# Kernel tuning notes

Measured on AMD Instinct MI355X. Metric: run time of the kernel, lower is better.

Reference implementation:

```python
import jax, jax.numpy as jnp
import numpy as np

DIM = 2048
HV = 32          # num value heads
HK = 16          # num key heads
DK = 128         # head_k_dim
DV = 128         # head_v_dim
KW = 4           # conv kernel width
KEY_DIM = HK * DK            # 2048
VAL_DIM = HV * DV            # 4096
CONV_DIM = 2 * KEY_DIM + VAL_DIM  # 8192
EPS = 1e-6
B, T = 2, 2048


def setup_inputs() -> dict:
    key = jax.random.key(0)
    ks = jax.random.split(key, 10)
    s = 0.02
    x = jax.random.normal(ks[0], (B, T, DIM), jnp.float32)
    W_qkv = jax.random.normal(ks[1], (DIM, CONV_DIM), jnp.float32) * s
    W_z = jax.random.normal(ks[2], (DIM, VAL_DIM), jnp.float32) * s
    W_a = jax.random.normal(ks[3], (DIM, HV), jnp.float32) * s
    W_b = jax.random.normal(ks[4], (DIM, HV), jnp.float32) * s
    W_out = jax.random.normal(ks[5], (VAL_DIM, DIM), jnp.float32) * s
    conv_w = jax.random.normal(ks[6], (CONV_DIM, KW), jnp.float32) * 0.2
    A_log = jnp.log(jax.random.uniform(ks[7], (HV,), jnp.float32, 1e-3, 16.0))
    dt_bias = jnp.ones((HV,), jnp.float32)
    norm_weight = jnp.ones((DV,), jnp.float32)
    return {"x": x, "W_qkv": W_qkv, "W_z": W_z, "W_a": W_a, "W_b": W_b,
            "W_out": W_out, "conv_w": conv_w, "dt_bias": dt_bias,
            "A_log": A_log, "norm_weight": norm_weight}


def _l2norm(t):
    return t * jax.lax.rsqrt(jnp.sum(t * t, axis=-1, keepdims=True) + EPS)


def _forward(x, W_qkv, W_z, W_a, W_b, W_out, conv_w, dt_bias, A_log, norm_weight):
    Bb, Tt, _ = x.shape
    mixed = x @ W_qkv                       # [B,T,CONV_DIM]
    z = x @ W_z                             # [B,T,VAL_DIM]
    a = x @ W_a                             # [B,T,HV]
    b = x @ W_b                             # [B,T,HV]

    # depthwise causal conv1d (left pad KW-1) + silu
    xp = jnp.pad(mixed, ((0, 0), (KW - 1, 0), (0, 0)))
    conv = sum(xp[:, i:i + Tt, :] * conv_w[:, i] for i in range(KW))
    mixed = jax.nn.silu(conv)

    q, k, v = jnp.split(mixed, [KEY_DIM, 2 * KEY_DIM], axis=-1)
    q = q.reshape(Bb, Tt, HK, DK)
    k = k.reshape(Bb, Tt, HK, DK)
    v = v.reshape(Bb, Tt, HV, DV)
    rep = HV // HK
    q = jnp.repeat(q, rep, axis=2)          # [B,T,HV,DK]
    k = jnp.repeat(k, rep, axis=2)

    # decay / beta
    beta = jax.nn.sigmoid(b)                                    # [B,T,HV]
    g = -jnp.exp(A_log) * jax.nn.softplus(a + dt_bias)          # [B,T,HV], < 0

    # qk l2norm in kernel + scale
    q = _l2norm(q) * (DK ** -0.5)
    k = _l2norm(k)

    # gated delta rule recurrence, time-major scan
    qT = q.transpose(1, 0, 2, 3)
    kT = k.transpose(1, 0, 2, 3)
    vT = v.transpose(1, 0, 2, 3)
    gT = g.transpose(1, 0, 2)
    bT = beta.transpose(1, 0, 2)
    S0 = jnp.zeros((Bb, HV, DK, DV), jnp.float32)

    def step(S, inp):
        qt, kt, vt, gt, bt = inp
        S = S * jnp.exp(gt)[..., None, None]
        pred = jnp.einsum('bhk,bhkv->bhv', kt, S)
        u = (vt - pred) * bt[..., None]
        S = S + jnp.einsum('bhk,bhv->bhkv', kt, u)
        o = jnp.einsum('bhk,bhkv->bhv', qt, S)
        return S, o

    _, oT = jax.lax.scan(step, S0, (qT, kT, vT, gT, bT))
    o = oT.transpose(1, 0, 2, 3)            # [B,T,HV,DV]

    # gated RMSNorm over head_v_dim: weight * rmsnorm(o) * silu(z)
    var = jnp.mean(o * o, axis=-1, keepdims=True)
    on = o * jax.lax.rsqrt(var + EPS) * norm_weight
    zg = z.reshape(Bb, Tt, HV, DV)
    on = on * jax.nn.silu(zg)

    return on.reshape(Bb, Tt, VAL_DIM) @ W_out


def reference(x, W_qkv, W_z, W_a, W_b, W_out, conv_w, dt_bias, A_log, norm_weight):
    return _forward(x, W_qkv, W_z, W_a, W_b, W_out, conv_w, dt_bias, A_log, norm_weight)
```

## Files before the change

### kernel.cpp

```cpp
#include <hip/hip_runtime.h>
#include <hip/hip_bf16.h>
#include <cstdint>
#include <cstddef>

#define DIM_ 2048
#define HV_ 32
#define HK_ 16
#define DK_ 128
#define DV_ 128
#define KW_ 4
#define KEY_DIM_ 2048
#define VAL_DIM_ 4096
#define CONV_DIM_ 8192
#define B_ 2
#define T_ 2048
#define BT_ 4096
#define CH_ 64
#define NC_ (T_ / CH_)

typedef short s8v __attribute__((ext_vector_type(8)));
typedef float f4v __attribute__((ext_vector_type(4)));

__device__ __forceinline__ unsigned short f2b(float f) {
    union { float f; unsigned u; } c; c.f = f;
    unsigned u = c.u;
    return (unsigned short)((u + 0x7fffu + ((u >> 16) & 1u)) >> 16);
}
__device__ __forceinline__ float b2f(unsigned short s) {
    union { unsigned u; float f; } c; c.u = ((unsigned)s) << 16;
    return c.f;
}
__device__ __forceinline__ unsigned int pk2(float a, float b) {
    return (unsigned)f2b(a) | ((unsigned)f2b(b) << 16);
}
__device__ __forceinline__ float silu(float x) { return x / (1.f + expf(-x)); }

__global__ void cast_bf16_k(const float* __restrict__ in, unsigned short* __restrict__ out, int n8) {
    int i = blockIdx.x * blockDim.x + threadIdx.x;
    if (i >= n8) return;
    int base = i * 8;
    f4v a = *(const f4v*)(in + base);
    f4v b = *(const f4v*)(in + base + 4);
    s8v o;
    o[0] = (short)f2b(a[0]); o[1] = (short)f2b(a[1]); o[2] = (short)f2b(a[2]); o[3] = (short)f2b(a[3]);
    o[4] = (short)f2b(b[0]); o[5] = (short)f2b(b[1]); o[6] = (short)f2b(b[2]); o[7] = (short)f2b(b[3]);
    *(s8v*)(out + base) = o;
}

__global__ void transpose_cast_k(const float* __restrict__ in, unsigned short* __restrict__ out,
                                 int R, int C) {
    __shared__ float tile[32][33];
    int c0 = blockIdx.x * 32, r0 = blockIdx.y * 32;
    int tx = threadIdx.x & 31, ty = threadIdx.x >> 5;
#pragma unroll
    for (int j = 0; j < 32; j += 8)
        tile[ty + j][tx] = in[(size_t)(r0 + ty + j) * C + c0 + tx];
    __syncthreads();
#pragma unroll
    for (int j = 0; j < 32; j += 8)
        out[(size_t)(c0 + ty + j) * R + r0 + tx] = f2b(tile[tx][ty + j]);
}

__global__ void pack_ab_k(const float* __restrict__ Wa, const float* __restrict__ Wb,
                          float* __restrict__ WabP) {
    int idx = blockIdx.x * 256 + threadIdx.x;
    int k = idx >> 6;
    int c = idx & 63;
    float v = (c < 32) ? Wa[(size_t)k * 32 + c] : Wb[(size_t)k * 32 + (c - 32)];
    WabP[((size_t)(k >> 2) * 64 + c) * 4 + (k & 3)] = v;
}

template <int OUT_BF16>
__global__ __launch_bounds__(256) void gemm_bt_k(const unsigned short* __restrict__ A,
                                                 const unsigned short* __restrict__ BT,
                                                 void* __restrict__ Cv,
                                                 int M, int N, int K) {
    __shared__ __attribute__((aligned(16))) unsigned short As[128 * 64];
    __shared__ __attribute__((aligned(16))) unsigned short Bs[128 * 64];
    const int tid = threadIdx.x;
    const int wid = tid >> 6, lane = tid & 63;
    const int wm = wid >> 1, wn = wid & 1;
    const int m0 = blockIdx.y * 128, n0 = blockIdx.x * 128;

    f4v acc[4][4];
#pragma unroll
    for (int i = 0; i < 4; i++)
#pragma unroll
        for (int j = 0; j < 4; j++) acc[i][j] = (f4v){0.f, 0.f, 0.f, 0.f};

    const int rowA = tid >> 3;
    const int cb   = (tid & 7) << 4;

    for (int kt = 0; kt < K; kt += 64) {
#pragma unroll
        for (int i = 0; i < 4; i++) {
            int row = i * 32 + rowA;
            int scb = cb ^ ((row & 7) << 4);
            const unsigned short* ga = A  + (size_t)(m0 + row) * K + kt + (scb >> 1);
            const unsigned short* gb = BT + (size_t)(n0 + row) * K + kt + (scb >> 1);
            char* la = (char*)As + i * 4096 + (wid << 10);
            char* lb = (char*)Bs + i * 4096 + (wid << 10);
            __builtin_amdgcn_global_load_lds(
                (const __attribute__((address_space(1))) unsigned int*)ga,
                (__attribute__((address_space(3))) unsigned int*)la, 16, 0, 0);
            __builtin_amdgcn_global_load_lds(
                (const __attribute__((address_space(1))) unsigned int*)gb,
                (__attribute__((address_space(3))) unsigned int*)lb, 16, 0, 0);
        }
        __syncthreads();
#pragma unroll
        for (int kk = 0; kk < 2; kk++) {
            s8v af[4], bfr[4];
#pragma unroll
            for (int mi = 0; mi < 4; mi++) {
                int row = wm * 64 + mi * 16 + (lane & 15);
                int byteoff = (row << 7) + ((kk * 64 + ((lane >> 4) << 4)) ^ ((row & 7) << 4));
                af[mi] = *(const s8v*)((const char*)As + byteoff);
            }
#pragma unroll
            for (int ni = 0; ni < 4; ni++) {
                int row = wn * 64 + ni * 16 + (lane & 15);
                int byteoff = (row << 7) + ((kk * 64 + ((lane >> 4) << 4)) ^ ((row & 7) << 4));
                bfr[ni] = *(const s8v*)((const char*)Bs + byteoff);
            }
#pragma unroll
            for (int mi = 0; mi < 4; mi++)
#pragma unroll
                for (int ni = 0; ni < 4; ni++)
                    acc[mi][ni] = __builtin_amdgcn_mfma_f32_16x16x32_bf16(
                        af[mi], bfr[ni], acc[mi][ni], 0, 0, 0);
        }
        __syncthreads();
    }
#pragma unroll
    for (int mi = 0; mi < 4; mi++) {
#pragma unroll
        for (int ni = 0; ni < 4; ni++) {
            int row = m0 + wm * 64 + mi * 16 + ((lane >> 4) << 2);
            int col = n0 + wn * 64 + ni * 16 + (lane & 15);
#pragma unroll
            for (int r = 0; r < 4; r++) {
                float v = acc[mi][ni][r];
                if (OUT_BF16)
                    ((unsigned short*)Cv)[(size_t)(row + r) * N + col] = f2b(v);
                else
                    ((float*)Cv)[(size_t)(row + r) * N + col] = v;
            }
        }
    }
}

__global__ __launch_bounds__(256) void ab_gbeta_k(const float* __restrict__ x,
                                                  const float* __restrict__ WabP,
                                                  const float* __restrict__ dt_bias,
                                                  const float* __restrict__ A_log,
                                                  float* __restrict__ g, float* __restrict__ beta) {
    const int c = threadIdx.x & 63;
    const int rg = __builtin_amdgcn_readfirstlane(threadIdx.x >> 6);
    const int row = blockIdx.x * 4 + rg;
    const float* xp = x + (size_t)row * 2048;
    const float* wp = WabP + c * 4;
    float acc0 = 0.f, acc1 = 0.f;
#pragma unroll 4
    for (int kb = 0; kb < 512; kb += 2) {
        f4v w0 = *(const f4v*)(wp + (size_t)kb * 256);
        f4v w1 = *(const f4v*)(wp + (size_t)(kb + 1) * 256);
        f4v x0 = *(const f4v*)(xp + kb * 4);
        f4v x1 = *(const f4v*)(xp + kb * 4 + 4);
        acc0 += x0[0] * w0[0] + x0[1] * w0[1] + x0[2] * w0[2] + x0[3] * w0[3];
        acc1 += x1[0] * w1[0] + x1[1] * w1[1] + x1[2] * w1[2] + x1[3] * w1[3];
    }
    float tot = acc0 + acc1;
    if (c < 32) {
        float av = tot + dt_bias[c];
        float sp = (av > 20.f) ? av : log1pf(expf(av));
        g[(size_t)row * 32 + c] = -expf(A_log[c]) * sp;
    } else {
        beta[(size_t)row * 32 + (c - 32)] = 1.f / (1.f + expf(-tot));
    }
}

__global__ __launch_bounds__(256) void conv_fused_k(const unsigned short* __restrict__ mixp,
                                                    const float* __restrict__ convw,
                                                    unsigned short* __restrict__ qn,
                                                    unsigned short* __restrict__ kn,
                                                    unsigned short* __restrict__ vv) {
    int btid = blockIdx.x;
    int t = btid & (T_ - 1);
    int c = (blockIdx.y << 9) + (threadIdx.x << 1);
    const unsigned short* base = mixp + (size_t)btid * CONV_DIM_ + c;
    unsigned m3 = *(const unsigned*)(base);
    unsigned m2 = (t >= 1) ? *(const unsigned*)(base - CONV_DIM_) : 0u;
    unsigned m1 = (t >= 2) ? *(const unsigned*)(base - 2 * CONV_DIM_) : 0u;
    unsigned m0 = (t >= 3) ? *(const unsigned*)(base - 3 * CONV_DIM_) : 0u;
    f4v w0 = *(const f4v*)(convw + (size_t)c * 4);
    f4v w1 = *(const f4v*)(convw + (size_t)c * 4 + 4);
    float v0 = b2f((unsigned short)(m3 & 0xffff)) * w0[3] + b2f((unsigned short)(m2 & 0xffff)) * w0[2]
             + b2f((unsigned short)(m1 & 0xffff)) * w0[1] + b2f((unsigned short)(m0 & 0xffff)) * w0[0];
    float v1 = b2f((unsigned short)(m3 >> 16)) * w1[3] + b2f((unsigned short)(m2 >> 16)) * w1[2]
             + b2f((unsigned short)(m1 >> 16)) * w1[1] + b2f((unsigned short)(m0 >> 16)) * w1[0];
    v0 = silu(v0); v1 = silu(v1);
    if (c < 2 * KEY_DIM_) {
        float ss = v0 * v0 + v1 * v1;
#pragma unroll
        for (int m = 1; m < 64; m <<= 1) ss += __shfl_xor(ss, m);
        float scale = rsqrtf(ss + 1e-6f);
        int head = (c >> 7) & 15, d = c & 127;
        if (c < KEY_DIM_) {
            scale *= 0.08838834764831845f;
            *(unsigned*)(qn + ((size_t)btid * HK_ + head) * DK_ + d) = pk2(v0 * scale, v1 * scale);
        } else {
            *(unsigned*)(kn + ((size_t)btid * HK_ + head) * DK_ + d) = pk2(v0 * scale, v1 * scale);
        }
    } else {
        *(unsigned*)(vv + (size_t)btid * VAL_DIM_ + (c - 2 * KEY_DIM_)) = pk2(v0, v1);
    }
}

__global__ __launch_bounds__(256) void chunk_pre_k(
    const unsigned short* __restrict__ qn, const unsigned short* __restrict__ kn,
    unsigned short* __restrict__ vv,
    const float* __restrict__ g, const float* __restrict__ beta,
    unsigned short* __restrict__ Wg, unsigned short* __restrict__ Aog,
    unsigned short* __restrict__ knT, float* __restrict__ expG, float* __restrict__ expGr)
{
    const int c = blockIdx.x, hp = blockIdx.y, b = blockIdx.z;
    const int tid = threadIdx.x, wid = tid >> 6, lane = tid & 63;
    const int r15 = lane & 15, g4 = lane >> 4;

    __shared__ __attribute__((aligned(16))) unsigned short Klds[64 * 128];
    __shared__ __attribute__((aligned(16))) unsigned short Xlds[128 * 64];
    __shared__ float AT[64][68];
    __shared__ float STmp[16][17];
    __shared__ float Gl2[2][64], Bl2[2][64], EG2[2][64];

    const size_t t0 = (size_t)b * T_ + (size_t)c * 64;

#pragma unroll
    for (int p = 0; p < 4; p++) {
        int row = p * 16 + (tid >> 4);
        int colB = (tid & 15) << 4;
        int sw = colB ^ ((row & 7) << 4);
        s8v kv = *(const s8v*)(kn + ((t0 + row) * HK_ + hp) * DK_ + (colB >> 1));
        *(s8v*)((char*)Klds + row * 256 + sw) = kv;
        s8v qv = *(const s8v*)(qn + ((t0 + row) * HK_ + hp) * DK_ + (colB >> 1));
        *(s8v*)((char*)Xlds + row * 256 + sw) = qv;
    }
    if (wid < 2) {
        int h = hp * 2 + wid;
        float v = g[(t0 + lane) * HV_ + h];
        float bv = beta[(t0 + lane) * HV_ + h];
#pragma unroll
        for (int off = 1; off < 64; off <<= 1) {
            float n = __shfl_up(v, off);
            if (lane >= off) v += n;
        }
        float Gn = __shfl(v, 63);
        float e1 = expf(v), e2 = expf(Gn - v);
        Gl2[wid][lane] = v;
        Bl2[wid][lane] = bv;
        EG2[wid][lane] = e1;
        size_t cbk = ((size_t)(b * 32 + h) * 32 + c);
        expG[cbk * 64 + lane] = e1;
        expGr[cbk * 64 + lane] = e2;
    }
    __syncthreads();

    f4v kkv[4], qkv[4];
#pragma unroll
    for (int jt = 0; jt < 4; jt++) { kkv[jt] = (f4v){0,0,0,0}; qkv[jt] = (f4v){0,0,0,0}; }
    const int arow = wid * 16 + r15;
#pragma unroll
    for (int ks = 0; ks < 4; ks++) {
        int abyte = arow * 256 + ((ks * 64 + (g4 << 4)) ^ ((arow & 7) << 4));
        s8v ak = *(const s8v*)((const char*)Klds + abyte);
        s8v aq = *(const s8v*)((const char*)Xlds + abyte);
#pragma unroll
        for (int jt = 0; jt < 4; jt++) {
            int jrow = jt * 16 + r15;
            int bbyte = jrow * 256 + ((ks * 64 + (g4 << 4)) ^ ((jrow & 7) << 4));
            s8v bk = *(const s8v*)((const char*)Klds + bbyte);
            kkv[jt] = __builtin_amdgcn_mfma_f32_16x16x32_bf16(ak, bk, kkv[jt], 0, 0, 0);
            qkv[jt] = __builtin_amdgcn_mfma_f32_16x16x32_bf16(aq, bk, qkv[jt], 0, 0, 0);
        }
    }

    for (int hh = 0; hh < 2; hh++) {
        const int h = hp * 2 + hh;
        const size_t cbk = ((size_t)(b * 32 + h) * 32 + c);

#pragma unroll
        for (int jt = 0; jt < 4; jt++) {
#pragma unroll
            for (int r = 0; r < 4; r++) {
                int i = wid * 16 + g4 * 4 + r;
                int j = jt * 16 + r15;
                float em = expf(fminf(Gl2[hh][i] - Gl2[hh][j], 0.f));
                AT[i][j] = (j < i) ? Bl2[hh][i] * em * kkv[jt][r] : 0.f;
                float ao = (j <= i) ? em * qkv[jt][r] : 0.f;
                Aog[cbk * 4096 + i * 64 + j] = f2b(ao);
            }
        }
        __syncthreads();

        for (int u = tid; u < 1024; u += 256) {
            int row = u >> 4, v0i = (u & 15) << 3;
            s8v vx = *(const s8v*)(vv + (t0 + row) * VAL_DIM_ + h * 128 + v0i);
            float bt = Bl2[hh][row];
#pragma unroll
            for (int e = 0; e < 8; e++) {
                int v = v0i + e;
                *(unsigned short*)((char*)Xlds + v * 128 + ((row * 2) ^ ((v & 7) << 4))) =
                    f2b(b2f((unsigned short)vx[e]) * bt);
            }
        }
        if (hh == 0) {
            int dk = tid & 127, th = (tid >> 7) << 5;
            size_t basek = ((size_t)(b * 16 + hp) * 128 + dk) * (size_t)T_ + (size_t)c * 64 + th;
#pragma unroll
            for (int t8 = 0; t8 < 4; t8++) {
                s8v kv;
#pragma unroll
                for (int e = 0; e < 8; e++) {
                    int tt = th + t8 * 8 + e;
                    kv[e] = (short)*(const unsigned short*)((const char*)Klds + tt * 256 + ((dk * 2) ^ ((tt & 7) << 4)));
                }
                *(s8v*)(knT + basek + t8 * 8) = kv;
            }
        }
        __syncthreads();

        if (lane < 16) {
            int r0 = wid * 16, col = lane;
#pragma unroll
            for (int i = 0; i < 16; i++) {
                float s = 0.f;
                for (int j = 0; j < i; j++) s += AT[r0 + i][r0 + j] * AT[r0 + j][r0 + col];
                AT[r0 + i][r0 + col] = ((col == i) ? 1.f : 0.f) - s;
            }
        }
        __syncthreads();

        {
            int ii = tid >> 4, jj = tid & 15;
            for (int I = 1; I < 4; I++)
                for (int J = 0; J < I; J++) {
                    float s = 0.f;
                    for (int K = J; K < I; K++) {
#pragma unroll
                        for (int m = 0; m < 16; m++)
                            s += AT[16 * I + ii][16 * K + m] * AT[16 * K + m][16 * J + jj];
                    }
                    STmp[ii][jj] = s;
                    __syncthreads();
                    float y = 0.f;
#pragma unroll
                    for (int m = 0; m < 16; m++) y += AT[16 * I + ii][16 * I + m] * STmp[m][jj];
                    __syncthreads();
                    AT[16 * I + ii][16 * J + jj] = -y;
                    __syncthreads();
                }
        }

        f4v tb[8];
#pragma unroll
        for (int vt = 0; vt < 8; vt++) tb[vt] = (f4v){0,0,0,0};
#pragma unroll
        for (int ks = 0; ks < 2; ks++) {
            s8v ta;
#pragma unroll
            for (int e = 0; e < 8; e++) ta[e] = (short)f2b(AT[arow][ks * 32 + g4 * 8 + e]);
#pragma unroll
            for (int vt = 0; vt < 8; vt++) {
                int v = vt * 16 + r15;
                int bbyte = v * 128 + ((ks * 64 + (g4 << 4)) ^ ((v & 7) << 4));
                s8v bv = *(const s8v*)((const char*)Xlds + bbyte);
                tb[vt] = __builtin_amdgcn_mfma_f32_16x16x32_bf16(ta, bv, tb[vt], 0, 0, 0);
            }
        }
#pragma unroll
        for (int vt = 0; vt < 8; vt++)
#pragma unroll
            for (int r = 0; r < 4; r++) {
                int i = wid * 16 + g4 * 4 + r, v = vt * 16 + r15;
                vv[(t0 + i) * VAL_DIM_ + h * 128 + v] = f2b(tb[vt][r]);
            }
        __syncthreads();

        {
            int dk = tid & 127;
            int tb0 = (tid >> 7) << 5;
#pragma unroll
            for (int t8 = 0; t8 < 4; t8++) {
                int tbase = tb0 + t8 * 8;
                s8v kw;
#pragma unroll
                for (int e = 0; e < 8; e++) {
                    int t = tbase + e;
                    float kv = b2f(*(const unsigned short*)((const char*)Klds + t * 256 + ((dk * 2) ^ ((t & 7) << 4))));
                    kw[e] = (short)f2b(kv * Bl2[hh][t] * EG2[hh][t]);
                }
                *(s8v*)((char*)Xlds + dk * 128 + ((tbase * 2) ^ ((dk & 7) << 4))) = kw;
            }
        }
        __syncthreads();

        f4v wm[8];
#pragma unroll
        for (int dt = 0; dt < 8; dt++) wm[dt] = (f4v){0,0,0,0};
#pragma unroll
        for (int ks = 0; ks < 2; ks++) {
            s8v ta;
#pragma unroll
            for (int e = 0; e < 8; e++) ta[e] = (short)f2b(AT[arow][ks * 32 + g4 * 8 + e]);
#pragma unroll
            for (int dt = 0; dt < 8; dt++) {
                int dkr = dt * 16 + r15;
                int bbyte = dkr * 128 + ((ks * 64 + (g4 << 4)) ^ ((dkr & 7) << 4));
                s8v bw = *(const s8v*)((const char*)Xlds + bbyte);
                wm[dt] = __builtin_amdgcn_mfma_f32_16x16x32_bf16(ta, bw, wm[dt], 0, 0, 0);
            }
        }
#pragma unroll
        for (int dt = 0; dt < 8; dt++)
#pragma unroll
            for (int r = 0; r < 4; r++) {
                int i = wid * 16 + g4 * 4 + r, dk = dt * 16 + r15;
                Wg[cbk * 8192 + i * 128 + dk] = f2b(wm[dt][r]);
            }
        __syncthreads();
    }
}

__global__ __launch_bounds__(256) void chunk_scan_k(
    const unsigned short* __restrict__ qn, const unsigned short* __restrict__ knT,
    const unsigned short* __restrict__ tbv,
    const unsigned short* __restrict__ Wg, const unsigned short* __restrict__ Aog,
    const float* __restrict__ expG, const float* __restrict__ expGr,
    unsigned short* __restrict__ ob)
{
    const int bx = blockIdx.x;
    const int vq = bx & 3, h = (bx >> 2) & 31, b = bx >> 7;
    const int hk = h >> 1;
    const int tid = threadIdx.x, wid = tid >> 6, lane = tid & 63;
    const int r15 = lane & 15, g4 = lane >> 4;

    __shared__ __attribute__((aligned(16))) unsigned short Slds[32 * 128];
    __shared__ __attribute__((aligned(16))) unsigned short Ulds[32 * 64];
    __shared__ __attribute__((aligned(16))) unsigned short Uplds[32 * 64];

    f4v S[2][2];
#pragma unroll
    for (int i = 0; i < 2; i++)
#pragma unroll
        for (int j = 0; j < 2; j++) S[i][j] = (f4v){0,0,0,0};

    struct ScanOps {
        s8v aw[4], aa[2], ak[4], q0[4];
        float tv[8], egr4[4], egi, gam;
    };
    ScanOps opA, opB;

    const unsigned short* kpbase = knT + ((size_t)(b * 16 + hk) * 128) * (size_t)T_;

    auto scan_load = [&](ScanOps& o, int c) {
        const size_t cbk = ((size_t)(b * 32 + h) * 32 + c);
        const size_t t0 = (size_t)b * T_ + (size_t)c * 64;
        const unsigned short* wp = Wg + cbk * 8192 + (size_t)(wid * 16 + r15) * 128;
#pragma unroll
        for (int ks = 0; ks < 4; ks++) o.aw[ks] = *(const s8v*)(wp + ks * 32 + g4 * 8);
        const unsigned short* ap = Aog + cbk * 4096 + (size_t)(wid * 16 + r15) * 64;
#pragma unroll
        for (int ks = 0; ks < 2; ks++) o.aa[ks] = *(const s8v*)(ap + ks * 32 + g4 * 8);
#pragma unroll
        for (int ks = 0; ks < 2; ks++)
#pragma unroll
            for (int dkt = 0; dkt < 2; dkt++)
                o.ak[ks * 2 + dkt] = *(const s8v*)(kpbase +
                    (size_t)((wid * 2 + dkt) * 16 + r15) * T_ + (size_t)c * 64 + ks * 32 + g4 * 8);
        const unsigned short* qp = qn + ((t0 + wid * 16 + r15) * HK_ + hk) * DK_;
#pragma unroll
        for (int ks = 0; ks < 4; ks++) o.q0[ks] = *(const s8v*)(qp + ks * 32 + g4 * 8);
#pragma unroll
        for (int vt = 0; vt < 2; vt++)
#pragma unroll
            for (int r = 0; r < 4; r++) {
                int t = wid * 16 + g4 * 4 + r;
                o.tv[vt * 4 + r] = b2f(tbv[(t0 + t) * VAL_DIM_ + h * 128 + vq * 32 + vt * 16 + r15]);
            }
#pragma unroll
        for (int r = 0; r < 4; r++) o.egr4[r] = expGr[cbk * 64 + wid * 16 + g4 * 4 + r];
        o.egi = expG[cbk * 64 + wid * 16 + r15];
        o.gam = expG[cbk * 64 + 63];
    };

    auto body = [&](ScanOps& o, int c) {
#pragma unroll
        for (int dkt = 0; dkt < 2; dkt++)
#pragma unroll
            for (int vt = 0; vt < 2; vt++) {
                int v = vt * 16 + r15;
                int dkb = ((wid * 2 + dkt) * 16 + g4 * 4) * 2;
                int sw = (v & 7) << 4;
                *(unsigned int*)((char*)Slds + v * 256 + ((dkb) ^ sw))     = pk2(S[dkt][vt][0], S[dkt][vt][1]);
                *(unsigned int*)((char*)Slds + v * 256 + ((dkb + 4) ^ sw)) = pk2(S[dkt][vt][2], S[dkt][vt][3]);
            }
        __syncthreads();

        f4v P[2]; P[0] = (f4v){0,0,0,0}; P[1] = (f4v){0,0,0,0};
        s8v sf[4][2];
#pragma unroll
        for (int ks = 0; ks < 4; ks++)
#pragma unroll
            for (int vt = 0; vt < 2; vt++) {
                int v = vt * 16 + r15;
                sf[ks][vt] = *(const s8v*)((const char*)Slds + v * 256 + ((ks * 64 + g4 * 16) ^ ((v & 7) << 4)));
                P[vt] = __builtin_amdgcn_mfma_f32_16x16x32_bf16(o.aw[ks], sf[ks][vt], P[vt], 0, 0, 0);
            }
#pragma unroll
        for (int vt = 0; vt < 2; vt++) {
            float uu[4], up[4];
#pragma unroll
            for (int r = 0; r < 4; r++) {
                uu[r] = o.tv[vt * 4 + r] - P[vt][r];
                up[r] = uu[r] * o.egr4[r];
            }
            int v = vt * 16 + r15;
            int tb2 = (wid * 16 + g4 * 4) * 2;
            int sw = (v & 7) << 4;
            *(unsigned int*)((char*)Ulds  + v * 128 + ((tb2) ^ sw))     = pk2(uu[0], uu[1]);
            *(unsigned int*)((char*)Ulds  + v * 128 + ((tb2 + 4) ^ sw)) = pk2(uu[2], uu[3]);
            *(unsigned int*)((char*)Uplds + v * 128 + ((tb2) ^ sw))     = pk2(up[0], up[1]);
            *(unsigned int*)((char*)Uplds + v * 128 + ((tb2 + 4) ^ sw)) = pk2(up[2], up[3]);
        }

        f4v O[2]; O[0] = (f4v){0,0,0,0}; O[1] = (f4v){0,0,0,0};
#pragma unroll
        for (int ks = 0; ks < 4; ks++) {
            s8v qg;
#pragma unroll
            for (int e = 0; e < 8; e++) qg[e] = (short)f2b(b2f((unsigned short)o.q0[ks][e]) * o.egi);
#pragma unroll
            for (int vt = 0; vt < 2; vt++)
                O[vt] = __builtin_amdgcn_mfma_f32_16x16x32_bf16(qg, sf[ks][vt], O[vt], 0, 0, 0);
        }
        __syncthreads();

#pragma unroll
        for (int ks = 0; ks < 2; ks++)
#pragma unroll
            for (int vt = 0; vt < 2; vt++) {
                int v = vt * 16 + r15;
                s8v bu = *(const s8v*)((const char*)Ulds + v * 128 + ((ks * 64 + g4 * 16) ^ ((v & 7) << 4)));
                O[vt] = __builtin_amdgcn_mfma_f32_16x16x32_bf16(o.aa[ks], bu, O[vt], 0, 0, 0);
            }
#pragma unroll
        for (int vt = 0; vt < 2; vt++)
#pragma unroll
            for (int r = 0; r < 4; r++) {
                int t = c * 64 + wid * 16 + g4 * 4 + r;
                ob[((size_t)b * T_ + t) * VAL_DIM_ + h * 128 + vq * 32 + vt * 16 + r15] = f2b(O[vt][r]);
            }

#pragma unroll
        for (int dkt = 0; dkt < 2; dkt++)
#pragma unroll
            for (int vt = 0; vt < 2; vt++) {
                S[dkt][vt][0] *= o.gam; S[dkt][vt][1] *= o.gam;
                S[dkt][vt][2] *= o.gam; S[dkt][vt][3] *= o.gam;
            }
#pragma unroll
        for (int ks = 0; ks < 2; ks++) {
            s8v bu[2];
#pragma unroll
            for (int vt = 0; vt < 2; vt++) {
                int v = vt * 16 + r15;
                bu[vt] = *(const s8v*)((const char*)Uplds + v * 128 + ((ks * 64 + g4 * 16) ^ ((v & 7) << 4)));
            }
#pragma unroll
            for (int dkt = 0; dkt < 2; dkt++)
#pragma unroll
                for (int vt = 0; vt < 2; vt++)
                    S[dkt][vt] = __builtin_amdgcn_mfma_f32_16x16x32_bf16(o.ak[ks * 2 + dkt], bu[vt], S[dkt][vt], 0, 0, 0);
        }
    };

    scan_load(opA, 0);
    for (int c = 0; c < NC_; c += 2) {
        scan_load(opB, (c + 1 < NC_) ? c + 1 : c);
        body(opA, c);
        if (c + 2 < NC_) scan_load(opA, c + 2);
        body(opB, c + 1);
    }
}

__global__ __launch_bounds__(256) void norm_gate_k(unsigned short* __restrict__ o,
                                                   const unsigned short* __restrict__ z,
                                                   const float* __restrict__ nw) {
    int lane = threadIdx.x & 63;
    size_t bh = (size_t)blockIdx.x * 4 + (threadIdx.x >> 6);
    unsigned ov = *(unsigned*)(o + bh * 128 + lane * 2);
    float v0 = b2f((unsigned short)(ov & 0xffff)), v1 = b2f((unsigned short)(ov >> 16));
    float ss = v0 * v0 + v1 * v1;
#pragma unroll
    for (int m = 1; m < 64; m <<= 1) ss += __shfl_xor(ss, m);
    float rr = rsqrtf(ss * (1.f / 128.f) + 1e-6f);
    unsigned zv = *(const unsigned*)(z + bh * 128 + lane * 2);
    float z0 = b2f((unsigned short)(zv & 0xffff)), z1 = b2f((unsigned short)(zv >> 16));
    float o0 = v0 * rr * nw[lane * 2]     * silu(z0);
    float o1 = v1 * rr * nw[lane * 2 + 1] * silu(z1);
    *(unsigned*)(o + bh * 128 + lane * 2) = pk2(o0, o1);
}

extern "C" void kernel_launch(void* const* d_in, const int* in_sizes, int n_in,
                              void* d_out, int out_size, void* d_ws, size_t ws_size,
                              hipStream_t stream) {
    const float* x      = (const float*)d_in[0];
    const float* W_qkv  = (const float*)d_in[1];
    const float* W_z    = (const float*)d_in[2];
    const float* W_a    = (const float*)d_in[3];
    const float* W_b    = (const float*)d_in[4];
    const float* W_out  = (const float*)d_in[5];
    const float* conv_w = (const float*)d_in[6];
    const float* dt_bias= (const float*)d_in[7];
    const float* A_log  = (const float*)d_in[8];
    const float* norm_w = (const float*)d_in[9];

    char* w = (char*)d_ws;
    const size_t MBc = (size_t)1 << 20;
    unsigned short* mixp  = (unsigned short*)(w);
    unsigned short* Wmat  = (unsigned short*)(w);
    unsigned short* knT   = (unsigned short*)(w + 32 * MBc);
    unsigned short* Aog   = (unsigned short*)(w + 48 * MBc);
    unsigned short* WqkvT = (unsigned short*)(w + 64 * MBc);
    unsigned short* obuf  = (unsigned short*)(w + 64 * MBc);
    unsigned short* kn    = (unsigned short*)(w + 80 * MBc);
    unsigned short* WzT   = (unsigned short*)(w + 96 * MBc);
    unsigned short* WoutT = (unsigned short*)(w + 96 * MBc);
    unsigned short* xb    = (unsigned short*)(w + 112 * MBc);
    unsigned short* qn    = (unsigned short*)(w + 112 * MBc);
    unsigned short* vv    = (unsigned short*)(w + 128 * MBc);
    unsigned short* zb    = (unsigned short*)(w + 160 * MBc);
    float* gbuf  = (float*)(w + 192 * MBc);
    float* bbuf  = (float*)(w + 192 * MBc + 512 * 1024);
    float* expG  = (float*)(w + 192 * MBc + 1024 * 1024);
    float* expGr = (float*)(w + 192 * MBc + 1536 * 1024);
    float* WabP  = (float*)(w + 194 * MBc);

    pack_ab_k<<<512, 256, 0, stream>>>(W_a, W_b, WabP);
    cast_bf16_k<<<(BT_ * DIM_ / 8 + 255) / 256, 256, 0, stream>>>(x, xb, BT_ * DIM_ / 8);
    ab_gbeta_k<<<BT_ / 4, 256, 0, stream>>>(x, WabP, dt_bias, A_log, gbuf, bbuf);
    transpose_cast_k<<<dim3(CONV_DIM_ / 32, DIM_ / 32), 256, 0, stream>>>(W_qkv, WqkvT, DIM_, CONV_DIM_);
    transpose_cast_k<<<dim3(VAL_DIM_ / 32, DIM_ / 32), 256, 0, stream>>>(W_z, WzT, DIM_, VAL_DIM_);
    gemm_bt_k<1><<<dim3(CONV_DIM_ / 128, BT_ / 128), 256, 0, stream>>>(xb, WqkvT, mixp, BT_, CONV_DIM_, DIM_);
    gemm_bt_k<1><<<dim3(VAL_DIM_ / 128, BT_ / 128), 256, 0, stream>>>(xb, WzT, zb, BT_, VAL_DIM_, DIM_);
    transpose_cast_k<<<dim3(DIM_ / 32, VAL_DIM_ / 32), 256, 0, stream>>>(W_out, WoutT, VAL_DIM_, DIM_);
    conv_fused_k<<<dim3(BT_, CONV_DIM_ / 512), 256, 0, stream>>>(mixp, conv_w, qn, kn, vv);
    chunk_pre_k<<<dim3(NC_, HV_ / 2, B_), 256, 0, stream>>>(qn, kn, vv, gbuf, bbuf,
                                                            Wmat, Aog, knT, expG, expGr);
    chunk_scan_k<<<B_ * HV_ * 4, 256, 0, stream>>>(qn, knT, vv, Wmat, Aog, expG, expGr, obuf);
    norm_gate_k<<<BT_ * HV_ / 4, 256, 0, stream>>>(obuf, zb, norm_w);
    gemm_bt_k<0><<<dim3(DIM_ / 128, BT_ / 128), 256, 0, stream>>>(obuf, WoutT, d_out, BT_, DIM_, VAL_DIM_);
}
```

Measured before the change: 699.5 us.

## Replace bf16 GEMM with 256x256 double-buffered 8-wave pipelined MFMA kernel

Replaces the 128x128 single-buffered GEMM with a 256x256-tile kernel using 512 threads and 128 KB of dynamic LDS split into two buffers. Global-to-LDS loads are broken into four stage units and interleaved with four MFMA sub-blocks per K step. Explicit vmcnt/lgkmcnt waits, barriers and s_setprio bracket the MFMA bursts so loads overlap compute. The larger tile raises reuse per LDS byte but cuts the block count, leaving the output projection with only 128 blocks, which may under-fill the GPU.

```diff
diff --git a/kernel.cpp b/kernel.cpp
--- a/kernel.cpp
+++ b/kernel.cpp
@@ -71,73 +71,138 @@
 }
 
 template <int OUT_BF16>
-__global__ __launch_bounds__(256) void gemm_bt_k(const unsigned short* __restrict__ A,
-                                                 const unsigned short* __restrict__ BT,
-                                                 void* __restrict__ Cv,
-                                                 int M, int N, int K) {
-    __shared__ __attribute__((aligned(16))) unsigned short As[128 * 64];
-    __shared__ __attribute__((aligned(16))) unsigned short Bs[128 * 64];
+__global__ __launch_bounds__(512) void gemm256_bt_k(const unsigned short* __restrict__ A,
+                                                    const unsigned short* __restrict__ BT,
+                                                    void* __restrict__ Cv,
+                                                    int M, int N, int K) {
+    extern __shared__ char lds[];
     const int tid = threadIdx.x;
     const int wid = tid >> 6, lane = tid & 63;
-    const int wm = wid >> 1, wn = wid & 1;
-    const int m0 = blockIdx.y * 128, n0 = blockIdx.x * 128;
-
-    f4v acc[4][4];
-#pragma unroll
-    for (int i = 0; i < 4; i++)
+    const int wm = wid >> 2, wn = wid & 3;
+    const int r15 = lane & 15, g4 = lane >> 4;
+    const int m0 = blockIdx.y * 256, n0 = blockIdx.x * 256;
+    const int NT = K >> 6;
+
+    f4v acc[8][4];
+#pragma unroll
+    for (int i = 0; i < 8; i++)
 #pragma unroll
         for (int j = 0; j < 4; j++) acc[i][j] = (f4v){0.f, 0.f, 0.f, 0.f};
 
-    const int rowA = tid >> 3;
-    const int cb   = (tid & 7) << 4;
-
-    for (int kt = 0; kt < K; kt += 64) {
-#pragma unroll
-        for (int i = 0; i < 4; i++) {
-            int row = i * 32 + rowA;
-            int scb = cb ^ ((row & 7) << 4);
-            const unsigned short* ga = A  + (size_t)(m0 + row) * K + kt + (scb >> 1);
-            const unsigned short* gb = BT + (size_t)(n0 + row) * K + kt + (scb >> 1);
-            char* la = (char*)As + i * 4096 + (wid << 10);
-            char* lb = (char*)Bs + i * 4096 + (wid << 10);
+    const int i8 = lane >> 3;
+    const int colb = (lane & 7) << 4;
+
+    auto stage = [&](int unit, int t) {
+        int buf = t & 1;
+        int matB = (unit == 1 || unit == 2);
+        int rs0;
+        if (unit == 0)      rs0 = wid * 8;
+        else if (unit == 3) rs0 = 64 + wid * 8;
+        else                rs0 = (wid < 4 ? wid * 8 : 64 + (wid - 4) * 8) + (unit == 2 ? 32 : 0);
+#pragma unroll
+        for (int p = 0; p < 2; p++) {
+            int rowst = rs0 + p * 128;
+            int row = rowst + i8;
+            int scol = colb ^ ((row & 7) << 4);
+            const unsigned short* g = (matB ? BT + (size_t)(n0 + row) * K
+                                            : A  + (size_t)(m0 + row) * K)
+                                      + t * 64 + (scol >> 1);
+            char* l = lds + buf * 65536 + matB * 32768 + rowst * 128;
             __builtin_amdgcn_global_load_lds(
-                (const __attribute__((address_space(1))) unsigned int*)ga,
-                (__attribute__((address_space(3))) unsigned int*)la, 16, 0, 0);
-            __builtin_amdgcn_global_load_lds(
-                (const __attribute__((address_space(1))) unsigned int*)gb,
-                (__attribute__((address_space(3))) unsigned int*)lb, 16, 0, 0);
-        }
-        __syncthreads();
-#pragma unroll
-        for (int kk = 0; kk < 2; kk++) {
-            s8v af[4], bfr[4];
-#pragma unroll
-            for (int mi = 0; mi < 4; mi++) {
-                int row = wm * 64 + mi * 16 + (lane & 15);
-                int byteoff = (row << 7) + ((kk * 64 + ((lane >> 4) << 4)) ^ ((row & 7) << 4));
-                af[mi] = *(const s8v*)((const char*)As + byteoff);
-            }
-#pragma unroll
-            for (int ni = 0; ni < 4; ni++) {
-                int row = wn * 64 + ni * 16 + (lane & 15);
-                int byteoff = (row << 7) + ((kk * 64 + ((lane >> 4) << 4)) ^ ((row & 7) << 4));
-                bfr[ni] = *(const s8v*)((const char*)Bs + byteoff);
-            }
-#pragma unroll
-            for (int mi = 0; mi < 4; mi++)
-#pragma unroll
-                for (int ni = 0; ni < 4; ni++)
-                    acc[mi][ni] = __builtin_amdgcn_mfma_f32_16x16x32_bf16(
-                        af[mi], bfr[ni], acc[mi][ni], 0, 0, 0);
-        }
-        __syncthreads();
-    }
-#pragma unroll
-    for (int mi = 0; mi < 4; mi++) {
+                (const __attribute__((address_space(1))) unsigned int*)g,
+                (__attribute__((address_space(3))) unsigned int*)l, 16, 0, 0);
+        }
+    };
+    auto loadA = [&](s8v* af, int mh, int buf) {
+        char* base = lds + buf * 65536;
+#pragma unroll
+        for (int mi = 0; mi < 4; mi++) {
+            int row = wm * 128 + mh * 64 + mi * 16 + r15;
+#pragma unroll
+            for (int kk = 0; kk < 2; kk++) {
+                int off = row * 128 + ((kk * 64 + g4 * 16) ^ ((row & 7) << 4));
+                af[mi * 2 + kk] = *(const s8v*)(base + off);
+            }
+        }
+    };
+    auto loadB = [&](s8v* bf, int nh, int buf) {
+        char* base = lds + buf * 65536 + 32768;
+#pragma unroll
+        for (int ni = 0; ni < 2; ni++) {
+            int row = wn * 64 + nh * 32 + ni * 16 + r15;
+#pragma unroll
+            for (int kk = 0; kk < 2; kk++) {
+                int off = row * 128 + ((kk * 64 + g4 * 16) ^ ((row & 7) << 4));
+                bf[ni * 2 + kk] = *(const s8v*)(base + off);
+            }
+        }
+    };
+    auto mfma16 = [&](s8v* af, s8v* bf, int mh, int nh) {
+#pragma unroll
+        for (int mi = 0; mi < 4; mi++)
+#pragma unroll
+            for (int ni = 0; ni < 2; ni++)
+#pragma unroll
+                for (int kk = 0; kk < 2; kk++)
+                    acc[mh * 4 + mi][nh * 2 + ni] = __builtin_amdgcn_mfma_f32_16x16x32_bf16(
+                        af[mi * 2 + kk], bf[ni * 2 + kk], acc[mh * 4 + mi][nh * 2 + ni], 0, 0, 0);
+    };
+
+    stage(0, 0); stage(1, 0); stage(2, 0); stage(3, 0);
+    stage(0, 1); stage(1, 1); stage(2, 1);
+    asm volatile("s_waitcnt vmcnt(6)" ::: "memory");
+    __builtin_amdgcn_s_barrier();
+
+    for (int u = 0; u < NT; u++) {
+        int buf = u & 1;
+        s8v afE[8], afO[8], bfE[4], bfO[4];
+
+        loadA(afE, 0, buf); loadB(bfE, 0, buf);
+        if (u + 1 < NT) stage(3, u + 1);
+        __builtin_amdgcn_s_barrier();
+        asm volatile("s_waitcnt lgkmcnt(0)" ::: "memory");
+        __builtin_amdgcn_sched_barrier(0);
+        __builtin_amdgcn_s_setprio(1);
+        mfma16(afE, bfE, 0, 0);
+        __builtin_amdgcn_s_setprio(0);
+        __builtin_amdgcn_s_barrier();
+
+        loadB(bfO, 1, buf);
+        if (u + 2 < NT) stage(0, u + 2);
+        __builtin_amdgcn_s_barrier();
+        asm volatile("s_waitcnt lgkmcnt(0)" ::: "memory");
+        __builtin_amdgcn_sched_barrier(0);
+        __builtin_amdgcn_s_setprio(1);
+        mfma16(afE, bfO, 0, 1);
+        __builtin_amdgcn_s_setprio(0);
+        __builtin_amdgcn_s_barrier();
+
+        loadA(afO, 1, buf);
+        if (u + 2 < NT) stage(1, u + 2);
+        __builtin_amdgcn_s_barrier();
+        asm volatile("s_waitcnt lgkmcnt(0)" ::: "memory");
+        __builtin_amdgcn_sched_barrier(0);
+        __builtin_amdgcn_s_setprio(1);
+        mfma16(afO, bfO, 1, 1);
+        __builtin_amdgcn_s_setprio(0);
+        __builtin_amdgcn_s_barrier();
+
+        if (u + 2 < NT) stage(2, u + 2);
+        __builtin_amdgcn_s_barrier();
+        __builtin_amdgcn_s_setprio(1);
+        mfma16(afO, bfE, 1, 0);
+        __builtin_amdgcn_s_setprio(0);
+        if (u == NT - 2) asm volatile("s_waitcnt vmcnt(0)" ::: "memory");
+        else             asm volatile("s_waitcnt vmcnt(6)" ::: "memory");
+        __builtin_amdgcn_s_barrier();
+    }
+
+#pragma unroll
+    for (int mi = 0; mi < 8; mi++)
 #pragma unroll
         for (int ni = 0; ni < 4; ni++) {
-            int row = m0 + wm * 64 + mi * 16 + ((lane >> 4) << 2);
-            int col = n0 + wn * 64 + ni * 16 + (lane & 15);
+            int row = m0 + wm * 128 + mi * 16 + g4 * 4;
+            int col = n0 + wn * 64 + ni * 16 + r15;
 #pragma unroll
             for (int r = 0; r < 4; r++) {
                 float v = acc[mi][ni][r];
@@ -147,7 +212,6 @@
                     ((float*)Cv)[(size_t)(row + r) * N + col] = v;
             }
         }
-    }
 }
 
 __global__ __launch_bounds__(256) void ab_gbeta_k(const float* __restrict__ x,
@@ -652,13 +716,13 @@
     ab_gbeta_k<<<BT_ / 4, 256, 0, stream>>>(x, WabP, dt_bias, A_log, gbuf, bbuf);
     transpose_cast_k<<<dim3(CONV_DIM_ / 32, DIM_ / 32), 256, 0, stream>>>(W_qkv, WqkvT, DIM_, CONV_DIM_);
     transpose_cast_k<<<dim3(VAL_DIM_ / 32, DIM_ / 32), 256, 0, stream>>>(W_z, WzT, DIM_, VAL_DIM_);
-    gemm_bt_k<1><<<dim3(CONV_DIM_ / 128, BT_ / 128), 256, 0, stream>>>(xb, WqkvT, mixp, BT_, CONV_DIM_, DIM_);
-    gemm_bt_k<1><<<dim3(VAL_DIM_ / 128, BT_ / 128), 256, 0, stream>>>(xb, WzT, zb, BT_, VAL_DIM_, DIM_);
+    gemm256_bt_k<1><<<dim3(CONV_DIM_ / 256, BT_ / 256), 512, 131072, stream>>>(xb, WqkvT, mixp, BT_, CONV_DIM_, DIM_);
+    gemm256_bt_k<1><<<dim3(VAL_DIM_ / 256, BT_ / 256), 512, 131072, stream>>>(xb, WzT, zb, BT_, VAL_DIM_, DIM_);
     transpose_cast_k<<<dim3(DIM_ / 32, VAL_DIM_ / 32), 256, 0, stream>>>(W_out, WoutT, VAL_DIM_, DIM_);
     conv_fused_k<<<dim3(BT_, CONV_DIM_ / 512), 256, 0, stream>>>(mixp, conv_w, qn, kn, vv);
     chunk_pre_k<<<dim3(NC_, HV_ / 2, B_), 256, 0, stream>>>(qn, kn, vv, gbuf, bbuf,
                                                             Wmat, Aog, knT, expG, expGr);
     chunk_scan_k<<<B_ * HV_ * 4, 256, 0, stream>>>(qn, knT, vv, Wmat, Aog, expG, expGr, obuf);
     norm_gate_k<<<BT_ * HV_ / 4, 256, 0, stream>>>(obuf, zb, norm_w);
-    gemm_bt_k<0><<<dim3(DIM_ / 128, BT_ / 128), 256, 0, stream>>>(obuf, WoutT, d_out, BT_, DIM_, VAL_DIM_);
-}
+    gemm256_bt_k<0><<<dim3(DIM_ / 256, BT_ / 256), 512, 131072, stream>>>(obuf, WoutT, d_out, BT_, DIM_, VAL_DIM_);
+}
```

After: 654.0 us. 1.07x faster.
